# Kernel tuning notes

Hardware: AMD Instinct MI355X
Metric: run time of the kernel (lower is better)

## Reference

```python
import jax, jax.numpy as jnp
import numpy as np

B, S, C = 2, 4096, 2048
H, D = 16, 128  # inner_dim = H*D = C
EPS = 1e-15     # processor self.eps
PAD_VAL = 1.0   # processor self.pad_val


def setup_inputs() -> dict:
    key = jax.random.key(0)
    ks = jax.random.split(key, 5)
    scale = C ** -0.5
    x = jax.random.normal(ks[0], (B, S, C), jnp.float32)
    Wq = jax.random.normal(ks[1], (C, C), jnp.float32) * scale
    Wk = jax.random.normal(ks[2], (C, C), jnp.float32) * scale
    Wv = jax.random.normal(ks[3], (C, C), jnp.float32) * scale
    Wo = jax.random.normal(ks[4], (C, C), jnp.float32) * scale
    bq = jnp.zeros((C,), jnp.float32)
    bk = jnp.zeros((C,), jnp.float32)
    bv = jnp.zeros((C,), jnp.float32)
    bo = jnp.zeros((C,), jnp.float32)
    # RoPE tables: pairs are adjacent (x.reshape(..., -1, 2)), so each freq repeats twice
    inv_freq = 1.0 / (10000.0 ** (np.arange(0, D, 2, dtype=np.float32) / D))
    freqs = np.outer(np.arange(S, dtype=np.float32), inv_freq)  # [S, D/2]
    emb = np.repeat(freqs, 2, axis=1)                            # [S, D]
    cos = jnp.asarray(np.cos(emb), jnp.float32)
    sin = jnp.asarray(np.sin(emb), jnp.float32)
    return {"x": x, "cos": cos, "sin": sin, "Wq": Wq, "bq": bq, "Wk": Wk,
            "bk": bk, "Wv": Wv, "bv": bv, "Wo": Wo, "bo": bo}


def _rope(t, cos, sin):
    # t: [B, H, S, D]; cos/sin: [S, D]; adjacent-pair rotation
    tr = t[..., 0::2]
    ti = t[..., 1::2]
    t_rot = jnp.stack([-ti, tr], axis=-1).reshape(t.shape)
    return t * cos + t_rot * sin


def reference(x, cos, sin, Wq, bq, Wk, bk, Wv, bv, Wo, bo):
    # projections -> [B, H, S, D] (matches transpose(-1,-2).reshape(B,H,D,S) split)
    q = (x @ Wq.T + bq).reshape(B, S, H, D).transpose(0, 2, 1, 3)
    k = (x @ Wk.T + bk).reshape(B, S, H, D).transpose(0, 2, 1, 3)
    v = (x @ Wv.T + bv).reshape(B, S, H, D).transpose(0, 2, 1, 3)
    # RoPE on q and k (self-attention), then ReLU feature map
    q = jax.nn.relu(_rope(q, cos, sin))
    k = jax.nn.relu(_rope(k, cos, sin))
    # pad value with ones along head_dim: torch F.pad(value,(0,0,0,1),value=1.0)
    v_pad = jnp.concatenate([v, jnp.full((B, H, S, 1), PAD_VAL, v.dtype)], axis=-1)  # [B,H,S,D+1]
    # linear attention: vk = value @ key  -> [B,H,D+1,D];  hs = vk @ query -> [B,H,D+1,S]
    vk = jnp.einsum('bhsn,bhsd->bhnd', v_pad, k)
    hs = jnp.einsum('bhnd,bhsd->bhns', vk, q)
    # eps-normalize by the padded-ones channel
    hs = hs[:, :, :-1] / (hs[:, :, -1:] + EPS)  # [B,H,D,S]
    out = hs.transpose(0, 3, 1, 2).reshape(B, S, H * D)  # view(B,H*D,S).permute(0,2,1)
    return out @ Wo.T + bo
```

## Files before the change

### kernel.cpp

```cpp
#include <hip/hip_runtime.h>


typedef unsigned short u16;
typedef __attribute__((ext_vector_type(8))) short bf16x8;
typedef __attribute__((ext_vector_type(4))) float f32x4;

__device__ __forceinline__ float bf2f(u16 u) {
    union { unsigned int i; float f; } x; x.i = ((unsigned int)u) << 16; return x.f;
}
__device__ __forceinline__ u16 f2bf(float f) {
    union { unsigned int i; float f; } x; x.f = f;
    unsigned int i = x.i;
    return (u16)((i + 0x7fffu + ((i >> 16) & 1u)) >> 16);
}
__device__ __forceinline__ uint4 pack8(const float* __restrict__ src) {
    float4 f0 = *(const float4*)(src);
    float4 f1 = *(const float4*)(src + 4);
    union { u16 u[8]; uint4 v; } P;
    P.u[0] = f2bf(f0.x); P.u[1] = f2bf(f0.y); P.u[2] = f2bf(f0.z); P.u[3] = f2bf(f0.w);
    P.u[4] = f2bf(f1.x); P.u[5] = f2bf(f1.y); P.u[6] = f2bf(f1.z); P.u[7] = f2bf(f1.w);
    return P.v;
}

__device__ __forceinline__ void gll16(void* lds, const void* g) {
    __builtin_amdgcn_global_load_lds(
        (const __attribute__((address_space(1))) unsigned int*)g,
        (__attribute__((address_space(3))) unsigned int*)lds, 16, 0, 0);
}

__global__ __launch_bounds__(256) void cast_bf16(const float* __restrict__ src,
                                                 u16* __restrict__ dst, int n8) {
    int i = blockIdx.x * 256 + threadIdx.x;
    if (i < n8) *(uint4*)(dst + (size_t)i * 8) = pack8(src + (size_t)i * 8);
}

__global__ __launch_bounds__(256) void gemm_qkv(
    const u16* __restrict__ Xb, const u16* __restrict__ Wqkvb,
    const float* __restrict__ bq, const float* __restrict__ bk, const float* __restrict__ bv,
    const float* __restrict__ cosT, const float* __restrict__ sinT,
    u16* __restrict__ Q, u16* __restrict__ K, u16* __restrict__ V)
{
    __shared__ __align__(16) u16 As[128 * 32];
    __shared__ __align__(16) u16 Bs[128 * 32];

    int t  = threadIdx.x;
    int bm = blockIdx.x;
    int bn = blockIdx.y;
    int region = bn >> 4;
    const u16*   W    = Wqkvb + (size_t)region * 4194304;
    const float* bias = (region == 0) ? bq : (region == 1 ? bk : bv);
    u16* OUT          = (region == 0) ? Q  : (region == 1 ? K  : V);

    int m0 = bm * 128;
    int n0 = (bn & 15) * 128;

    int w = t >> 6, lane = t & 63, quad = lane >> 4, l16 = lane & 15;
    int wm0 = (w >> 1) * 64, wn0 = (w & 1) * 64;
    int w32 = w * 32;
    int lr  = lane >> 2;
    int lc  = (lane & 3) * 8;

    const u16* ga = Xb + (size_t)(m0 + w32 + lr) * 2048 + lc;
    const u16* gb = W  + (size_t)(n0 + w32 + lr) * 2048 + lc;

    f32x4 acc[4][4] = {};

    for (int k0 = 0; k0 < 2048; k0 += 32) {
        __syncthreads();
        gll16(As + (size_t)w32 * 32,        ga + k0);
        gll16(As + (size_t)(w32 + 16) * 32, ga + k0 + 16 * 2048);
        gll16(Bs + (size_t)w32 * 32,        gb + k0);
        gll16(Bs + (size_t)(w32 + 16) * 32, gb + k0 + 16 * 2048);
        __syncthreads();

        bf16x8 af[4], bfr[4];
#pragma unroll
        for (int i = 0; i < 4; i++) af[i]  = *(const bf16x8*)(As + (wm0 + i * 16 + l16) * 32 + quad * 8);
#pragma unroll
        for (int j = 0; j < 4; j++) bfr[j] = *(const bf16x8*)(Bs + (wn0 + j * 16 + l16) * 32 + quad * 8);
#pragma unroll
        for (int i = 0; i < 4; i++)
#pragma unroll
            for (int j = 0; j < 4; j++)
                acc[i][j] = __builtin_amdgcn_mfma_f32_16x16x32_bf16(af[i], bfr[j], acc[i][j], 0, 0, 0);
    }

#pragma unroll
    for (int i = 0; i < 4; i++) {
#pragma unroll
        for (int j = 0; j < 4; j++) {
            int nc   = n0 + wn0 + j * 16 + l16;
            int h    = nc >> 7, dpos = nc & 127;
            float bia = bias[nc];
#pragma unroll
            for (int r = 0; r < 4; r++) {
                int mr = m0 + wm0 + i * 16 + quad * 4 + r;
                int b  = mr >> 12, s = mr & 4095;
                float val = acc[i][j][r] + bia;
                if (region < 2) {
                    float pair = __shfl_xor(val, 1, 64);
                    float c  = cosT[s * 128 + dpos];
                    float sn = sinT[s * 128 + dpos];
                    val = fmaxf(val * c + ((dpos & 1) ? pair : -pair) * sn, 0.f);
                }
                OUT[((size_t)(b * 16 + h) * 4096 + s) * 128 + dpos] = f2bf(val);
            }
        }
    }
}

__global__ __launch_bounds__(256) void vk_partial(
    const u16* __restrict__ Kb, const u16* __restrict__ Vb, float* __restrict__ part)
{
    int bh = blockIdx.x;
    int sp = blockIdx.y;
    int t  = threadIdx.x;
    int tn = t >> 4, td = t & 15;
    int n0 = tn * 8, d0 = td * 8;
    const u16* Kp = Kb + (size_t)bh * 4096 * 128;
    const u16* Vp = Vb + (size_t)bh * 4096 * 128;
    int s0 = sp * 512;

    __shared__ __align__(16) u16 ks[8 * 128];
    __shared__ __align__(16) u16 vs[8 * 128];

    float acc[8][8] = {};
    float ksum[8] = {};

    for (int sc = 0; sc < 512; sc += 8) {
        __syncthreads();
        {
            int tt   = t & 127;
            int row  = tt >> 4;
            int cole = (tt & 15) * 8;
            const u16* srcp = (t < 128) ? Kp : Vp;
            u16*       dstp = (t < 128) ? ks : vs;
            const u16* src = srcp + (size_t)(s0 + sc + row) * 128 + cole;
            *(uint4*)((char*)dstp + tt * 16) = *(const uint4*)src;
        }
        __syncthreads();
#pragma unroll
        for (int ss = 0; ss < 8; ss++) {
            float vv[8], kv[8];
#pragma unroll
            for (int j = 0; j < 8; j++) vv[j] = bf2f(vs[ss * 128 + n0 + j]);
#pragma unroll
            for (int j = 0; j < 8; j++) kv[j] = bf2f(ks[ss * 128 + d0 + j]);
#pragma unroll
            for (int i = 0; i < 8; i++)
#pragma unroll
                for (int j = 0; j < 8; j++) acc[i][j] += vv[i] * kv[j];
            if (tn == 0) {
#pragma unroll
                for (int j = 0; j < 8; j++) ksum[j] += kv[j];
            }
        }
    }

    float* dst = part + (size_t)(bh * 8 + sp) * 16512;
#pragma unroll
    for (int i = 0; i < 8; i++)
#pragma unroll
        for (int j = 0; j < 8; j++) dst[(n0 + i) * 128 + d0 + j] = acc[i][j];
    if (tn == 0) {
#pragma unroll
        for (int j = 0; j < 8; j++) dst[16384 + d0 + j] = ksum[j];
    }
}

__global__ __launch_bounds__(256) void vk_reduce(const float* __restrict__ part,
                                                 float* __restrict__ vkf)
{
    int bh = blockIdx.x;
    int by = blockIdx.y;
    int t  = threadIdx.x;
    int end = (by + 1) * 2064;
    for (int idx = by * 2064 + t; idx < end; idx += 256) {
        float s = 0.f;
#pragma unroll
        for (int p = 0; p < 8; p++) s += part[(size_t)(bh * 8 + p) * 16512 + idx];
        vkf[(size_t)bh * 16512 + idx] = s;
    }
}

__global__ __launch_bounds__(256) void den_kernel(
    const u16* __restrict__ Qb, const float* __restrict__ vkf, float* __restrict__ rden)
{
    int bh = blockIdx.x, sb = blockIdx.y;
    __shared__ float ksumL[128];
    int t = threadIdx.x;
    if (t < 128) ksumL[t] = vkf[(size_t)bh * 16512 + 16384 + t];
    __syncthreads();
    int srow = t >> 1, half = t & 1;
    const u16*  q   = Qb + ((size_t)bh * 4096 + sb * 128 + srow) * 128 + half * 64;
    const float* kp = ksumL + half * 64;
    float p = 0.f;
#pragma unroll 8
    for (int d = 0; d < 64; d += 4) {
        ushort4 qv = *(const ushort4*)(q + d);
        p += bf2f(qv.x) * kp[d] + bf2f(qv.y) * kp[d + 1]
           + bf2f(qv.z) * kp[d + 2] + bf2f(qv.w) * kp[d + 3];
    }
    p += __shfl_xor(p, 1, 64);
    if (half == 0) rden[(size_t)bh * 4096 + sb * 128 + srow] = 1.0f / (p + 1e-15f);
}

__global__ __launch_bounds__(256) void hs_mfma(
    const u16* __restrict__ Qb, const float* __restrict__ vkf,
    const float* __restrict__ rden, u16* __restrict__ HS)
{
    int bh = blockIdx.x, sc = blockIdx.y;
    __shared__ __align__(16) u16 qL[128 * 136];
    __shared__ __align__(16) u16 vkL[128 * 136];
    __shared__ float rdL[128];
    int t = threadIdx.x;

    const u16*   Qp   = Qb + ((size_t)bh * 4096 + sc * 128) * 128;
    const float* vsrc = vkf + (size_t)bh * 16512;
    int row = t >> 4, colc = (t & 15) * 8;
#pragma unroll
    for (int r8 = 0; r8 < 8; r8++) {
        int rr = row + r8 * 16;
        *(uint4*)(qL  + rr * 136 + colc) = *(const uint4*)(Qp + (size_t)rr * 128 + colc);
        *(uint4*)(vkL + rr * 136 + colc) = pack8(vsrc + (size_t)rr * 128 + colc);
    }
    if (t < 128) rdL[t] = rden[(size_t)bh * 4096 + sc * 128 + t];
    __syncthreads();

    int w = t >> 6, lane = t & 63, quad = lane >> 4, l16 = lane & 15;
    int wm0 = (w >> 1) * 64, wn0 = (w & 1) * 64;
    f32x4 acc[4][4] = {};
#pragma unroll
    for (int ks = 0; ks < 4; ks++) {
        bf16x8 af[4], bfr[4];
#pragma unroll
        for (int i = 0; i < 4; i++) af[i]  = *(const bf16x8*)(qL  + (wm0 + i * 16 + l16) * 136 + ks * 32 + quad * 8);
#pragma unroll
        for (int j = 0; j < 4; j++) bfr[j] = *(const bf16x8*)(vkL + (wn0 + j * 16 + l16) * 136 + ks * 32 + quad * 8);
#pragma unroll
        for (int i = 0; i < 4; i++)
#pragma unroll
            for (int j = 0; j < 4; j++)
                acc[i][j] = __builtin_amdgcn_mfma_f32_16x16x32_bf16(af[i], bfr[j], acc[i][j], 0, 0, 0);
    }

    int b = bh >> 4, h = bh & 15;
#pragma unroll
    for (int i = 0; i < 4; i++) {
#pragma unroll
        for (int j = 0; j < 4; j++) {
#pragma unroll
            for (int r = 0; r < 4; r++) {
                int sl = wm0 + i * 16 + quad * 4 + r;
                int n  = wn0 + j * 16 + l16;
                size_t srow = (size_t)b * 4096 + sc * 128 + sl;
                HS[srow * 2048 + h * 128 + n] = f2bf(acc[i][j][r] * rdL[sl]);
            }
        }
    }
}

__global__ __launch_bounds__(256) void gemm_out(
    const u16* __restrict__ HSm, const u16* __restrict__ Wob,
    const float* __restrict__ bo, float* __restrict__ OUT)
{
    __shared__ __align__(16) u16 As[128 * 32];
    __shared__ __align__(16) u16 Bs[128 * 32];

    int t  = threadIdx.x;
    int m0 = blockIdx.x * 128;
    int n0 = blockIdx.y * 128;

    int w = t >> 6, lane = t & 63, quad = lane >> 4, l16 = lane & 15;
    int wm0 = (w >> 1) * 64, wn0 = (w & 1) * 64;
    int w32 = w * 32;
    int lr  = lane >> 2;
    int lc  = (lane & 3) * 8;

    const u16* ga = HSm + (size_t)(m0 + w32 + lr) * 2048 + lc;
    const u16* gb = Wob + (size_t)(n0 + w32 + lr) * 2048 + lc;

    f32x4 acc[4][4] = {};

    for (int k0 = 0; k0 < 2048; k0 += 32) {
        __syncthreads();
        gll16(As + (size_t)w32 * 32,        ga + k0);
        gll16(As + (size_t)(w32 + 16) * 32, ga + k0 + 16 * 2048);
        gll16(Bs + (size_t)w32 * 32,        gb + k0);
        gll16(Bs + (size_t)(w32 + 16) * 32, gb + k0 + 16 * 2048);
        __syncthreads();

        bf16x8 af[4], bfr[4];
#pragma unroll
        for (int i = 0; i < 4; i++) af[i]  = *(const bf16x8*)(As + (wm0 + i * 16 + l16) * 32 + quad * 8);
#pragma unroll
        for (int j = 0; j < 4; j++) bfr[j] = *(const bf16x8*)(Bs + (wn0 + j * 16 + l16) * 32 + quad * 8);
#pragma unroll
        for (int i = 0; i < 4; i++)
#pragma unroll
            for (int j = 0; j < 4; j++)
                acc[i][j] = __builtin_amdgcn_mfma_f32_16x16x32_bf16(af[i], bfr[j], acc[i][j], 0, 0, 0);
    }

#pragma unroll
    for (int i = 0; i < 4; i++) {
#pragma unroll
        for (int j = 0; j < 4; j++) {
            int nc = n0 + wn0 + j * 16 + l16;
            float bia = bo[nc];
#pragma unroll
            for (int r = 0; r < 4; r++) {
                int mr = m0 + wm0 + i * 16 + quad * 4 + r;
                OUT[(size_t)mr * 2048 + nc] = acc[i][j][r] + bia;
            }
        }
    }
}

extern "C" void kernel_launch(void* const* d_in, const int* in_sizes, int n_in,
                              void* d_out, int out_size, void* d_ws, size_t ws_size,
                              hipStream_t stream) {
    const float* x    = (const float*)d_in[0];
    const float* cosT = (const float*)d_in[1];
    const float* sinT = (const float*)d_in[2];
    const float* Wq   = (const float*)d_in[3];
    const float* bq   = (const float*)d_in[4];
    const float* Wk   = (const float*)d_in[5];
    const float* bk   = (const float*)d_in[6];
    const float* Wv   = (const float*)d_in[7];
    const float* bv   = (const float*)d_in[8];
    const float* Wo   = (const float*)d_in[9];
    const float* bo   = (const float*)d_in[10];

    char* ws = (char*)d_ws;
    u16*   Wqkvb = (u16*)(ws);
    u16*   Wob   = (u16*)(ws + 25165824);
    u16*   Xb    = (u16*)(ws + 33554432);
    float* part  = (float*)(ws + 33554432);
    u16*   V     = (u16*)(ws + 67108864);
    u16*   HS    = V;
    float* vkf   = (float*)(ws + 100663296);
    float* rden  = (float*)(ws + 102776832);

    u16* Q  = (u16*)d_out;
    u16* Kb = (u16*)d_out + 16777216;

    cast_bf16<<<8192, 256, 0, stream>>>(x,  Xb, 2097152);
    cast_bf16<<<2048, 256, 0, stream>>>(Wq, Wqkvb,           524288);
    cast_bf16<<<2048, 256, 0, stream>>>(Wk, Wqkvb + 4194304, 524288);
    cast_bf16<<<2048, 256, 0, stream>>>(Wv, Wqkvb + 8388608, 524288);
    cast_bf16<<<2048, 256, 0, stream>>>(Wo, Wob, 524288);

    gemm_qkv<<<dim3(64, 48), 256, 0, stream>>>(Xb, Wqkvb, bq, bk, bv, cosT, sinT, Q, Kb, V);
    vk_partial<<<dim3(32, 8), 256, 0, stream>>>(Kb, V, part);
    vk_reduce<<<dim3(32, 8), 256, 0, stream>>>(part, vkf);
    den_kernel<<<dim3(32, 32), 256, 0, stream>>>(Q, vkf, rden);
    hs_mfma<<<dim3(32, 32), 256, 0, stream>>>(Q, vkf, rden, HS);
    gemm_out<<<dim3(64, 16), 256, 0, stream>>>(HS, Wob, bo, (float*)d_out);
}
```

Measured before the change: 668.5 us.

## Use MFMA for V·K reduction, fuse casts, fold denominator into hs kernel, deepen GEMM k-step

Replaces the scalar FMA vk_partial kernel with an MFMA-based kernel that transposes K/V tiles into swizzled LDS, and computes the key-sum in a separate atomic kernel. The five cast launches are merged into one, and the denominator computation is folded into hs_mfma. The QKV and output GEMMs load two 32-wide k-slices per barrier pair, halving synchronisation count. This adds a memset and atomics, and uses more LDS in the GEMMs.

```diff
diff --git a/kernel.cpp b/kernel.cpp
--- a/kernel.cpp
+++ b/kernel.cpp
@@ -21,17 +21,26 @@
     P.u[4] = f2bf(f1.x); P.u[5] = f2bf(f1.y); P.u[6] = f2bf(f1.z); P.u[7] = f2bf(f1.w);
     return P.v;
 }
-
 __device__ __forceinline__ void gll16(void* lds, const void* g) {
     __builtin_amdgcn_global_load_lds(
         (const __attribute__((address_space(1))) unsigned int*)g,
         (__attribute__((address_space(3))) unsigned int*)lds, 16, 0, 0);
 }
 
-__global__ __launch_bounds__(256) void cast_bf16(const float* __restrict__ src,
-                                                 u16* __restrict__ dst, int n8) {
-    int i = blockIdx.x * 256 + threadIdx.x;
-    if (i < n8) *(uint4*)(dst + (size_t)i * 8) = pack8(src + (size_t)i * 8);
+__global__ __launch_bounds__(256) void cast_all(
+    const float* __restrict__ x,  const float* __restrict__ Wq,
+    const float* __restrict__ Wk, const float* __restrict__ Wv,
+    const float* __restrict__ Wo,
+    u16* __restrict__ Xb, u16* __restrict__ Wqkvb, u16* __restrict__ Wob)
+{
+    int bid = blockIdx.x, t = threadIdx.x;
+    const float* s; u16* d; size_t i;
+    if (bid < 8192)       { s = x;  d = Xb;              i = (size_t)bid * 256 + t; }
+    else if (bid < 10240) { s = Wq; d = Wqkvb;           i = (size_t)(bid - 8192)  * 256 + t; }
+    else if (bid < 12288) { s = Wk; d = Wqkvb + 4194304; i = (size_t)(bid - 10240) * 256 + t; }
+    else if (bid < 14336) { s = Wv; d = Wqkvb + 8388608; i = (size_t)(bid - 12288) * 256 + t; }
+    else                  { s = Wo; d = Wob;             i = (size_t)(bid - 14336) * 256 + t; }
+    *(uint4*)(d + i * 8) = pack8(s + i * 8);
 }
 
 __global__ __launch_bounds__(256) void gemm_qkv(
@@ -40,8 +49,8 @@
     const float* __restrict__ cosT, const float* __restrict__ sinT,
     u16* __restrict__ Q, u16* __restrict__ K, u16* __restrict__ V)
 {
-    __shared__ __align__(16) u16 As[128 * 32];
-    __shared__ __align__(16) u16 Bs[128 * 32];
+    __shared__ __align__(16) u16 As[2 * 128 * 32];
+    __shared__ __align__(16) u16 Bs[2 * 128 * 32];
 
     int t  = threadIdx.x;
     int bm = blockIdx.x;
@@ -65,24 +74,30 @@
 
     f32x4 acc[4][4] = {};
 
-    for (int k0 = 0; k0 < 2048; k0 += 32) {
-        __syncthreads();
-        gll16(As + (size_t)w32 * 32,        ga + k0);
-        gll16(As + (size_t)(w32 + 16) * 32, ga + k0 + 16 * 2048);
-        gll16(Bs + (size_t)w32 * 32,        gb + k0);
-        gll16(Bs + (size_t)(w32 + 16) * 32, gb + k0 + 16 * 2048);
-        __syncthreads();
-
-        bf16x8 af[4], bfr[4];
-#pragma unroll
-        for (int i = 0; i < 4; i++) af[i]  = *(const bf16x8*)(As + (wm0 + i * 16 + l16) * 32 + quad * 8);
-#pragma unroll
-        for (int j = 0; j < 4; j++) bfr[j] = *(const bf16x8*)(Bs + (wn0 + j * 16 + l16) * 32 + quad * 8);
-#pragma unroll
-        for (int i = 0; i < 4; i++)
-#pragma unroll
-            for (int j = 0; j < 4; j++)
-                acc[i][j] = __builtin_amdgcn_mfma_f32_16x16x32_bf16(af[i], bfr[j], acc[i][j], 0, 0, 0);
+    for (int k0 = 0; k0 < 2048; k0 += 64) {
+        __syncthreads();
+#pragma unroll
+        for (int p = 0; p < 2; p++) {
+            gll16(As + p * 4096 + (size_t)w32 * 32,        ga + k0 + p * 32);
+            gll16(As + p * 4096 + (size_t)(w32 + 16) * 32, ga + k0 + p * 32 + 16 * 2048);
+            gll16(Bs + p * 4096 + (size_t)w32 * 32,        gb + k0 + p * 32);
+            gll16(Bs + p * 4096 + (size_t)(w32 + 16) * 32, gb + k0 + p * 32 + 16 * 2048);
+        }
+        __syncthreads();
+
+#pragma unroll
+        for (int kk = 0; kk < 2; kk++) {
+            bf16x8 af[4], bfr[4];
+#pragma unroll
+            for (int i = 0; i < 4; i++) af[i]  = *(const bf16x8*)(As + kk * 4096 + (wm0 + i * 16 + l16) * 32 + quad * 8);
+#pragma unroll
+            for (int j = 0; j < 4; j++) bfr[j] = *(const bf16x8*)(Bs + kk * 4096 + (wn0 + j * 16 + l16) * 32 + quad * 8);
+#pragma unroll
+            for (int i = 0; i < 4; i++)
+#pragma unroll
+                for (int j = 0; j < 4; j++)
+                    acc[i][j] = __builtin_amdgcn_mfma_f32_16x16x32_bf16(af[i], bfr[j], acc[i][j], 0, 0, 0);
+        }
     }
 
 #pragma unroll
@@ -109,114 +124,135 @@
     }
 }
 
-__global__ __launch_bounds__(256) void vk_partial(
+__global__ __launch_bounds__(256) void ksum_kernel(
+    const u16* __restrict__ Kb, float* __restrict__ ksumbuf)
+{
+    int bh = blockIdx.x, sc8 = blockIdx.y, t = threadIdx.x;
+    int dpair = (t & 63) * 2, sq = t >> 6;
+    const u16* base = Kb + (size_t)bh * 524288 + (size_t)(sc8 * 512 + sq * 128) * 128 + dpair;
+    float s0 = 0.f, s1 = 0.f;
+#pragma unroll 8
+    for (int r = 0; r < 128; r++) {
+        unsigned int wv = *(const unsigned int*)(base + (size_t)r * 128);
+        s0 += bf2f((u16)(wv & 0xffff));
+        s1 += bf2f((u16)(wv >> 16));
+    }
+    __shared__ float red[4][128];
+    red[sq][dpair]     = s0;
+    red[sq][dpair + 1] = s1;
+    __syncthreads();
+    if (t < 128) {
+        float tot = red[0][t] + red[1][t] + red[2][t] + red[3][t];
+        atomicAdd(&ksumbuf[bh * 128 + t], tot);
+    }
+}
+
+__device__ __forceinline__ int vkswz(int r, int s) {
+    return r * 32 + (((( s >> 3) + (r >> 3)) & 3) << 3) + (s & 7);
+}
+
+__global__ __launch_bounds__(256) void vk_mfma(
     const u16* __restrict__ Kb, const u16* __restrict__ Vb, float* __restrict__ part)
 {
     int bh = blockIdx.x;
-    int sp = blockIdx.y;
+    int sk = blockIdx.y;
     int t  = threadIdx.x;
-    int tn = t >> 4, td = t & 15;
-    int n0 = tn * 8, d0 = td * 8;
-    const u16* Kp = Kb + (size_t)bh * 4096 * 128;
-    const u16* Vp = Vb + (size_t)bh * 4096 * 128;
-    int s0 = sp * 512;
-
-    __shared__ __align__(16) u16 ks[8 * 128];
-    __shared__ __align__(16) u16 vs[8 * 128];
-
-    float acc[8][8] = {};
-    float ksum[8] = {};
-
-    for (int sc = 0; sc < 512; sc += 8) {
+    int s0 = sk * 512;
+
+    __shared__ __align__(16) u16 Kt[128 * 32];
+    __shared__ __align__(16) u16 Vt[128 * 32];
+
+    const u16* Kp = Kb + (size_t)bh * 524288;
+    const u16* Vp = Vb + (size_t)bh * 524288;
+
+    int dgrp  = t & 15;
+    int d0    = dgrp * 8;
+    int spair = (t >> 4) * 2;
+    int sg    = spair >> 3;
+
+    int w = t >> 6, lane = t & 63, quad = lane >> 4, l16 = lane & 15;
+    int nbase = (w >> 1) * 64, dbase = (w & 1) * 64;
+
+    f32x4 acc[4][4] = {};
+
+    for (int tile = 0; tile < 16; tile++) {
+        int st = s0 + tile * 32;
         __syncthreads();
         {
-            int tt   = t & 127;
-            int row  = tt >> 4;
-            int cole = (tt & 15) * 8;
-            const u16* srcp = (t < 128) ? Kp : Vp;
-            u16*       dstp = (t < 128) ? ks : vs;
-            const u16* src = srcp + (size_t)(s0 + sc + row) * 128 + cole;
-            *(uint4*)((char*)dstp + tt * 16) = *(const uint4*)src;
-        }
-        __syncthreads();
-#pragma unroll
-        for (int ss = 0; ss < 8; ss++) {
-            float vv[8], kv[8];
-#pragma unroll
-            for (int j = 0; j < 8; j++) vv[j] = bf2f(vs[ss * 128 + n0 + j]);
-#pragma unroll
-            for (int j = 0; j < 8; j++) kv[j] = bf2f(ks[ss * 128 + d0 + j]);
-#pragma unroll
-            for (int i = 0; i < 8; i++)
-#pragma unroll
-                for (int j = 0; j < 8; j++) acc[i][j] += vv[i] * kv[j];
-            if (tn == 0) {
-#pragma unroll
-                for (int j = 0; j < 8; j++) ksum[j] += kv[j];
+            const u16* kg = Kp + (size_t)(st + spair) * 128 + d0;
+            const u16* vg = Vp + (size_t)(st + spair) * 128 + d0;
+            union { uint4 v; u16 u[8]; } ka, kb, va, vb;
+            ka.v = *(const uint4*)kg;  kb.v = *(const uint4*)(kg + 128);
+            va.v = *(const uint4*)vg;  vb.v = *(const uint4*)(vg + 128);
+            int swz = (((sg + dgrp) & 3) << 3) + (spair & 7);
+#pragma unroll
+            for (int i = 0; i < 8; i++) {
+                int e = (d0 + i) * 32 + swz;
+                *(unsigned int*)(Kt + e) = (unsigned int)ka.u[i] | ((unsigned int)kb.u[i] << 16);
+                *(unsigned int*)(Vt + e) = (unsigned int)va.u[i] | ((unsigned int)vb.u[i] << 16);
             }
         }
-    }
-
-    float* dst = part + (size_t)(bh * 8 + sp) * 16512;
-#pragma unroll
-    for (int i = 0; i < 8; i++)
-#pragma unroll
-        for (int j = 0; j < 8; j++) dst[(n0 + i) * 128 + d0 + j] = acc[i][j];
-    if (tn == 0) {
-#pragma unroll
-        for (int j = 0; j < 8; j++) dst[16384 + d0 + j] = ksum[j];
+        __syncthreads();
+
+        bf16x8 af[4], bfr[4];
+#pragma unroll
+        for (int i = 0; i < 4; i++) {
+            int r = nbase + i * 16 + l16;
+            af[i] = *(const bf16x8*)(Vt + r * 32 + (((quad + (r >> 3)) & 3) << 3));
+        }
+#pragma unroll
+        for (int j = 0; j < 4; j++) {
+            int r = dbase + j * 16 + l16;
+            bfr[j] = *(const bf16x8*)(Kt + r * 32 + (((quad + (r >> 3)) & 3) << 3));
+        }
+#pragma unroll
+        for (int i = 0; i < 4; i++)
+#pragma unroll
+            for (int j = 0; j < 4; j++)
+                acc[i][j] = __builtin_amdgcn_mfma_f32_16x16x32_bf16(af[i], bfr[j], acc[i][j], 0, 0, 0);
+    }
+
+    float* dst = part + (size_t)(bh * 8 + sk) * 16384;
+#pragma unroll
+    for (int i = 0; i < 4; i++) {
+#pragma unroll
+        for (int j = 0; j < 4; j++) {
+#pragma unroll
+            for (int r = 0; r < 4; r++) {
+                int n = nbase + i * 16 + quad * 4 + r;
+                int d = dbase + j * 16 + l16;
+                dst[n * 128 + d] = acc[i][j][r];
+            }
+        }
     }
 }
 
 __global__ __launch_bounds__(256) void vk_reduce(const float* __restrict__ part,
                                                  float* __restrict__ vkf)
 {
-    int bh = blockIdx.x;
-    int by = blockIdx.y;
-    int t  = threadIdx.x;
-    int end = (by + 1) * 2064;
-    for (int idx = by * 2064 + t; idx < end; idx += 256) {
+    int bh = blockIdx.x, by = blockIdx.y, t = threadIdx.x;
+    int end = (by + 1) * 2048;
+    for (int idx = by * 2048 + t; idx < end; idx += 256) {
         float s = 0.f;
 #pragma unroll
-        for (int p = 0; p < 8; p++) s += part[(size_t)(bh * 8 + p) * 16512 + idx];
-        vkf[(size_t)bh * 16512 + idx] = s;
-    }
-}
-
-__global__ __launch_bounds__(256) void den_kernel(
-    const u16* __restrict__ Qb, const float* __restrict__ vkf, float* __restrict__ rden)
-{
-    int bh = blockIdx.x, sb = blockIdx.y;
-    __shared__ float ksumL[128];
-    int t = threadIdx.x;
-    if (t < 128) ksumL[t] = vkf[(size_t)bh * 16512 + 16384 + t];
-    __syncthreads();
-    int srow = t >> 1, half = t & 1;
-    const u16*  q   = Qb + ((size_t)bh * 4096 + sb * 128 + srow) * 128 + half * 64;
-    const float* kp = ksumL + half * 64;
-    float p = 0.f;
-#pragma unroll 8
-    for (int d = 0; d < 64; d += 4) {
-        ushort4 qv = *(const ushort4*)(q + d);
-        p += bf2f(qv.x) * kp[d] + bf2f(qv.y) * kp[d + 1]
-           + bf2f(qv.z) * kp[d + 2] + bf2f(qv.w) * kp[d + 3];
-    }
-    p += __shfl_xor(p, 1, 64);
-    if (half == 0) rden[(size_t)bh * 4096 + sb * 128 + srow] = 1.0f / (p + 1e-15f);
+        for (int p = 0; p < 8; p++) s += part[(size_t)(bh * 8 + p) * 16384 + idx];
+        vkf[(size_t)bh * 16384 + idx] = s;
+    }
 }
 
 __global__ __launch_bounds__(256) void hs_mfma(
     const u16* __restrict__ Qb, const float* __restrict__ vkf,
-    const float* __restrict__ rden, u16* __restrict__ HS)
+    const float* __restrict__ ksumbuf, u16* __restrict__ HS)
 {
     int bh = blockIdx.x, sc = blockIdx.y;
     __shared__ __align__(16) u16 qL[128 * 136];
     __shared__ __align__(16) u16 vkL[128 * 136];
     __shared__ float rdL[128];
+    __shared__ float ksumL[128];
     int t = threadIdx.x;
 
     const u16*   Qp   = Qb + ((size_t)bh * 4096 + sc * 128) * 128;
-    const float* vsrc = vkf + (size_t)bh * 16512;
+    const float* vsrc = vkf + (size_t)bh * 16384;
     int row = t >> 4, colc = (t & 15) * 8;
 #pragma unroll
     for (int r8 = 0; r8 < 8; r8++) {
@@ -224,8 +260,23 @@
         *(uint4*)(qL  + rr * 136 + colc) = *(const uint4*)(Qp + (size_t)rr * 128 + colc);
         *(uint4*)(vkL + rr * 136 + colc) = pack8(vsrc + (size_t)rr * 128 + colc);
     }
-    if (t < 128) rdL[t] = rden[(size_t)bh * 4096 + sc * 128 + t];
+    if (t < 128) ksumL[t] = ksumbuf[bh * 128 + t];
     __syncthreads();
+
+    {
+        int srow = t >> 1, half = t & 1;
+        const u16*   q  = qL + srow * 136 + half * 64;
+        const float* kp = ksumL + half * 64;
+        float p = 0.f;
+#pragma unroll 8
+        for (int d = 0; d < 64; d += 4) {
+            ushort4 qv = *(const ushort4*)(q + d);
+            p += bf2f(qv.x) * kp[d] + bf2f(qv.y) * kp[d + 1]
+               + bf2f(qv.z) * kp[d + 2] + bf2f(qv.w) * kp[d + 3];
+        }
+        p += __shfl_xor(p, 1, 64);
+        if (half == 0) rdL[srow] = 1.0f / (p + 1e-15f);
+    }
 
     int w = t >> 6, lane = t & 63, quad = lane >> 4, l16 = lane & 15;
     int wm0 = (w >> 1) * 64, wn0 = (w & 1) * 64;
@@ -243,6 +294,7 @@
             for (int j = 0; j < 4; j++)
                 acc[i][j] = __builtin_amdgcn_mfma_f32_16x16x32_bf16(af[i], bfr[j], acc[i][j], 0, 0, 0);
     }
+    __syncthreads();
 
     int b = bh >> 4, h = bh & 15;
 #pragma unroll
@@ -264,8 +316,8 @@
     const u16* __restrict__ HSm, const u16* __restrict__ Wob,
     const float* __restrict__ bo, float* __restrict__ OUT)
 {
-    __shared__ __align__(16) u16 As[128 * 32];
-    __shared__ __align__(16) u16 Bs[128 * 32];
+    __shared__ __align__(16) u16 As[2 * 128 * 32];
+    __shared__ __align__(16) u16 Bs[2 * 128 * 32];
 
     int t  = threadIdx.x;
     int m0 = blockIdx.x * 128;
@@ -282,24 +334,30 @@
 
     f32x4 acc[4][4] = {};
 
-    for (int k0 = 0; k0 < 2048; k0 += 32) {
-        __syncthreads();
-        gll16(As + (size_t)w32 * 32,        ga + k0);
-        gll16(As + (size_t)(w32 + 16) * 32, ga + k0 + 16 * 2048);
-        gll16(Bs + (size_t)w32 * 32,        gb + k0);
-        gll16(Bs + (size_t)(w32 + 16) * 32, gb + k0 + 16 * 2048);
-        __syncthreads();
-
-        bf16x8 af[4], bfr[4];
-#pragma unroll
-        for (int i = 0; i < 4; i++) af[i]  = *(const bf16x8*)(As + (wm0 + i * 16 + l16) * 32 + quad * 8);
-#pragma unroll
-        for (int j = 0; j < 4; j++) bfr[j] = *(const bf16x8*)(Bs + (wn0 + j * 16 + l16) * 32 + quad * 8);
-#pragma unroll
-        for (int i = 0; i < 4; i++)
-#pragma unroll
-            for (int j = 0; j < 4; j++)
-                acc[i][j] = __builtin_amdgcn_mfma_f32_16x16x32_bf16(af[i], bfr[j], acc[i][j], 0, 0, 0);
+    for (int k0 = 0; k0 < 2048; k0 += 64) {
+        __syncthreads();
+#pragma unroll
+        for (int p = 0; p < 2; p++) {
+            gll16(As + p * 4096 + (size_t)w32 * 32,        ga + k0 + p * 32);
+            gll16(As + p * 4096 + (size_t)(w32 + 16) * 32, ga + k0 + p * 32 + 16 * 2048);
+            gll16(Bs + p * 4096 + (size_t)w32 * 32,        gb + k0 + p * 32);
+            gll16(Bs + p * 4096 + (size_t)(w32 + 16) * 32, gb + k0 + p * 32 + 16 * 2048);
+        }
+        __syncthreads();
+
+#pragma unroll
+        for (int kk = 0; kk < 2; kk++) {
+            bf16x8 af[4], bfr[4];
+#pragma unroll
+            for (int i = 0; i < 4; i++) af[i]  = *(const bf16x8*)(As + kk * 4096 + (wm0 + i * 16 + l16) * 32 + quad * 8);
+#pragma unroll
+            for (int j = 0; j < 4; j++) bfr[j] = *(const bf16x8*)(Bs + kk * 4096 + (wn0 + j * 16 + l16) * 32 + quad * 8);
+#pragma unroll
+            for (int i = 0; i < 4; i++)
+#pragma unroll
+                for (int j = 0; j < 4; j++)
+                    acc[i][j] = __builtin_amdgcn_mfma_f32_16x16x32_bf16(af[i], bfr[j], acc[i][j], 0, 0, 0);
+        }
     }
 
 #pragma unroll
@@ -333,28 +391,24 @@
     const float* bo   = (const float*)d_in[10];
 
     char* ws = (char*)d_ws;
-    u16*   Wqkvb = (u16*)(ws);
-    u16*   Wob   = (u16*)(ws + 25165824);
-    u16*   Xb    = (u16*)(ws + 33554432);
-    float* part  = (float*)(ws + 33554432);
-    u16*   V     = (u16*)(ws + 67108864);
-    u16*   HS    = V;
-    float* vkf   = (float*)(ws + 100663296);
-    float* rden  = (float*)(ws + 102776832);
+    u16*   Wqkvb   = (u16*)(ws);
+    u16*   Wob     = (u16*)(ws + 25165824);
+    u16*   Xb      = (u16*)(ws + 33554432);
+    float* part    = (float*)(ws + 33554432);
+    u16*   V       = (u16*)(ws + 67108864);
+    u16*   HS      = V;
+    float* vkf     = (float*)(ws + 100663296);
+    float* ksumbuf = (float*)(ws + 102760448);
 
     u16* Q  = (u16*)d_out;
     u16* Kb = (u16*)d_out + 16777216;
 
-    cast_bf16<<<8192, 256, 0, stream>>>(x,  Xb, 2097152);
-    cast_bf16<<<2048, 256, 0, stream>>>(Wq, Wqkvb,           524288);
-    cast_bf16<<<2048, 256, 0, stream>>>(Wk, Wqkvb + 4194304, 524288);
-    cast_bf16<<<2048, 256, 0, stream>>>(Wv, Wqkvb + 8388608, 524288);
-    cast_bf16<<<2048, 256, 0, stream>>>(Wo, Wob, 524288);
-
+    hipMemsetAsync(ksumbuf, 0, 32 * 128 * sizeof(float), stream);
+    cast_all<<<16384, 256, 0, stream>>>(x, Wq, Wk, Wv, Wo, Xb, Wqkvb, Wob);
     gemm_qkv<<<dim3(64, 48), 256, 0, stream>>>(Xb, Wqkvb, bq, bk, bv, cosT, sinT, Q, Kb, V);
-    vk_partial<<<dim3(32, 8), 256, 0, stream>>>(Kb, V, part);
+    ksum_kernel<<<dim3(32, 8), 256, 0, stream>>>(Kb, ksumbuf);
+    vk_mfma<<<dim3(32, 8), 256, 0, stream>>>(Kb, V, part);
     vk_reduce<<<dim3(32, 8), 256, 0, stream>>>(part, vkf);
-    den_kernel<<<dim3(32, 32), 256, 0, stream>>>(Q, vkf, rden);
-    hs_mfma<<<dim3(32, 32), 256, 0, stream>>>(Q, vkf, rden, HS);
+    hs_mfma<<<dim3(32, 32), 256, 0, stream>>>(Q, vkf, ksumbuf, HS);
     gemm_out<<<dim3(64, 16), 256, 0, stream>>>(HS, Wob, bo, (float*)d_out);
 }
```

After: 587.3 us. 1.14x faster.
